# Kernel optimization log

Measured on AMD Instinct MI355X. Metric: run time of the kernel, lower is better.

## Reference

```python
import jax, jax.numpy as jnp
from jax import lax
import numpy as np

B, T, H, A, C = 32, 4096, 512, 512, 32  # batch, enc frames, hidden, attn_size, conv_size


def setup_inputs() -> dict:
    key = jax.random.key(0)
    ks = jax.random.split(key, 10)
    return {
        "decoder_output": jax.random.normal(ks[0], (B, 1, H), jnp.float32),
        "encoder_outputs": jax.random.normal(ks[1], (B, T, H), jnp.float32),
        "last_alignment": jax.random.uniform(ks[2], (B, T), jnp.float32),
        "conv_w": jax.random.normal(ks[3], (C, 1, 3), jnp.float32) * 0.1,   # Conv1d(1->C, k=3)
        "conv_b": jax.random.normal(ks[4], (C,), jnp.float32) * 0.1,
        "W": jax.random.normal(ks[5], (A, H), jnp.float32) * (1.0 / np.sqrt(H)),
        "V": jax.random.normal(ks[6], (A, H), jnp.float32) * (1.0 / np.sqrt(H)),
        "U": jax.random.normal(ks[7], (A, C), jnp.float32) * (1.0 / np.sqrt(C)),
        "b": jax.random.uniform(ks[8], (A,), jnp.float32, -0.1, 0.1),
        "w": jax.random.normal(ks[9], (A,), jnp.float32) * (1.0 / np.sqrt(A)),
    }


def reference(decoder_output, encoder_outputs, last_alignment, conv_w, conv_b, W, V, U, b, w):
    # location conv: [B,1,T] -> [B,C,T], kernel 3, padding 1
    conv = lax.conv_general_dilated(
        last_alignment[:, None, :], conv_w,
        window_strides=(1,), padding=[(1, 1)],
        dimension_numbers=("NCH", "OIH", "NCH"))
    conv_feat = (conv + conv_b[None, :, None]).transpose(0, 2, 1)  # [B,T,C]

    dec_proj = jnp.einsum("blh,ah->bla", decoder_output, W)        # [B,1,A]
    enc_proj = jnp.einsum("bth,ah->bta", encoder_outputs, V)       # [B,T,A]
    loc_proj = jnp.einsum("btc,ac->bta", conv_feat, U)             # [B,T,A]

    scores = jnp.einsum("bta,a->bt", jnp.tanh(dec_proj + enc_proj + loc_proj + b), w)  # [B,T]
    alignment = jax.nn.softmax(scores, axis=-1)                    # [B,T]
    output = jnp.einsum("bt,bth->bh", alignment, encoder_outputs)  # [B,H]
    return output, alignment
```

## Files before the change

### kernel.cpp

```cpp
#include <hip/hip_runtime.h>
#include <hip/hip_bf16.h>

#define B_ 32
#define T_ 4096
#define H_ 512
#define A_ 512
#define C_ 32
#define KTOT 544
#define NKS  (KTOT / 32)
#define TT   128

typedef float f32x4 __attribute__((ext_vector_type(4)));
typedef __bf16 bf16x8 __attribute__((ext_vector_type(8)));
typedef __bf16 bf16x4 __attribute__((ext_vector_type(4)));

__device__ inline float fast_tanh(float x) {
    float t = __expf(2.0f * x);
    return 1.0f - 2.0f / (t + 1.0f);
}

__device__ __forceinline__ void async16(const void* g, void* l) {
    __builtin_amdgcn_global_load_lds(
        (const __attribute__((address_space(1))) unsigned int*)g,
        (__attribute__((address_space(3))) unsigned int*)l, 16, 0, 0);
}

__global__ __launch_bounds__(256) void prep_kernel(
    const float* __restrict__ dec, const float* __restrict__ W,
    const float* __restrict__ bvec, const float* __restrict__ V,
    const float* __restrict__ U,
    float* __restrict__ dpb, __bf16* __restrict__ Vsall) {
    int id = blockIdx.x * 256 + threadIdx.x;
    const int N1 = B_ * A_;
    const int N2 = A_ * H_;
    if (id < N1) {
        int b = id / A_, a = id % A_;
        const float* dr = dec + b * H_;
        const float* wr = W + (size_t)a * H_;
        float s = 0.f;
        #pragma unroll 8
        for (int h = 0; h < H_; ++h) s += dr[h] * wr[h];
        dpb[id] = s + bvec[a];
    } else if (id < N1 + N2) {
        int e = id - N1;
        int a = e >> 9, k = e & 511;
        Vsall[((k >> 3) * A_ + a) * 8 + (k & 7)] = (__bf16)V[(size_t)a * H_ + k];
    } else {
        int e = id - N1 - N2;
        int a = e >> 5, c = e & 31;
        int k = H_ + c;
        Vsall[((k >> 3) * A_ + a) * 8 + (k & 7)] = (__bf16)U[a * C_ + c];
    }
}

__global__ __launch_bounds__(1024) void scores_mfma(
    const float* __restrict__ enc, const float* __restrict__ align,
    const float* __restrict__ conv_w, const float* __restrict__ conv_b,
    const __bf16* __restrict__ Vsall, const float* __restrict__ dpb,
    const float* __restrict__ wvec, float* __restrict__ scores) {
    const int t0 = blockIdx.x * TT;
    const int b  = blockIdx.y;
    const int tid = threadIdx.x;
    const int lane = tid & 63, wid = tid >> 6;
    const int row0 = lane & 15;
    const int kg   = lane >> 4;
    const int wq   = wid & 3;
    const int wr   = wid >> 2;
    const int wcol = wq * 128;

    __shared__ char smem[114688];
    float* spart = (float*)smem;

    const float* encb = enc + ((size_t)b * T_ + t0) * H_;
    const int arow = tid >> 3;
    const int akq  = tid & 7;
    const int aswz = ((arow >> 1) & 3) << 1;
    const int awbyte = arow * 64 + ((akq ^ aswz) << 3);

    int arbyte[2];
    #pragma unroll
    for (int m = 0; m < 2; ++m) {
        int row = wr * 32 + m * 16 + row0;
        int rs = ((row >> 1) & 3) << 1;
        arbyte[m] = row * 64 + (((kg << 1) ^ rs) << 3);
    }

    f32x4 areg[2];
    float cx0 = 0.f, cx1 = 0.f, cx2 = 0.f;

    #pragma unroll
    for (int s = 0; s < 2; ++s) {
        char* bdst = smem + 16384 + s * 32768;
        #pragma unroll
        for (int i = 0; i < 2; ++i) {
            int u = i * 1024 + tid;
            async16(Vsall + (size_t)s * 16384 + (size_t)u * 8, bdst + u * 16);
        }
    }
    {
        f32x4 a0 = *reinterpret_cast<const f32x4*>(encb + arow * H_ + akq * 4);
        areg[1]  = *reinterpret_cast<const f32x4*>(encb + arow * H_ + 32 + akq * 4);
        bf16x4 v;
        v[0] = (__bf16)a0.x; v[1] = (__bf16)a0.y; v[2] = (__bf16)a0.z; v[3] = (__bf16)a0.w;
        *reinterpret_cast<bf16x4*>(smem + awbyte) = v;
    }
    asm volatile("s_waitcnt vmcnt(0) lgkmcnt(0)" ::: "memory");
    __builtin_amdgcn_sched_barrier(0);
    __builtin_amdgcn_s_barrier();

    f32x4 acc[2][8];
    #pragma unroll
    for (int m = 0; m < 2; ++m)
        #pragma unroll
        for (int n = 0; n < 8; ++n) acc[m][n] = (f32x4){0.f, 0.f, 0.f, 0.f};

    #pragma unroll
    for (int ks = 0; ks < NKS; ++ks) {
        if (ks + 2 <= NKS - 1) {
            char* bdst = smem + 16384 + ((ks + 2) % 3) * 32768;
            const __bf16* src = Vsall + (size_t)(ks + 2) * 16384;
            #pragma unroll
            for (int i = 0; i < 2; ++i) {
                int u = i * 1024 + tid;
                async16(src + (size_t)u * 8, bdst + u * 16);
            }
            if (ks + 2 < NKS - 1) {
                areg[ks & 1] = *reinterpret_cast<const f32x4*>(
                    encb + arow * H_ + (ks + 2) * 32 + akq * 4);
            } else {
                int t = t0 + arow;
                int tm = (t > 0) ? t - 1 : 0;
                int tp = (t + 1 < T_) ? t + 1 : T_ - 1;
                cx0 = align[(size_t)b * T_ + tm];
                cx1 = align[(size_t)b * T_ + t];
                cx2 = align[(size_t)b * T_ + tp];
                if (t == 0) cx0 = 0.f;
                if (t + 1 == T_) cx2 = 0.f;
            }
        }

        char* Ard = smem + (ks & 1) * 8192;
        bf16x8 afrag[2];
        #pragma unroll
        for (int m = 0; m < 2; ++m)
            afrag[m] = *reinterpret_cast<const bf16x8*>(Ard + arbyte[m]);
        const __bf16* bp = (const __bf16*)(smem + 16384 + (ks % 3) * 32768) + kg * (A_ * 8);
        #pragma unroll
        for (int n = 0; n < 8; ++n) {
            bf16x8 bfrag = *reinterpret_cast<const bf16x8*>(bp + (wcol + n * 16 + row0) * 8);
            acc[0][n] = __builtin_amdgcn_mfma_f32_16x16x32_bf16(afrag[0], bfrag, acc[0][n], 0, 0, 0);
            acc[1][n] = __builtin_amdgcn_mfma_f32_16x16x32_bf16(afrag[1], bfrag, acc[1][n], 0, 0, 0);
        }

        if (ks + 1 <= NKS - 1) {
            bf16x4 v;
            if (ks + 1 < NKS - 1) {
                f32x4 a = areg[(ks + 1) & 1];
                v[0] = (__bf16)a.x; v[1] = (__bf16)a.y; v[2] = (__bf16)a.z; v[3] = (__bf16)a.w;
            } else {
                #pragma unroll
                for (int e = 0; e < 4; ++e) {
                    int c = akq * 4 + e;
                    v[e] = (__bf16)(conv_b[c] + conv_w[c * 3] * cx0
                                  + conv_w[c * 3 + 1] * cx1 + conv_w[c * 3 + 2] * cx2);
                }
            }
            char* Adst = smem + ((ks + 1) & 1) * 8192;
            *reinterpret_cast<bf16x4*>(Adst + awbyte) = v;
        }

        if (ks < 14) {
            asm volatile("s_waitcnt vmcnt(3) lgkmcnt(0)" ::: "memory");
        } else if (ks == 14) {
            asm volatile("s_waitcnt vmcnt(5) lgkmcnt(0)" ::: "memory");
        } else if (ks == 15) {
            asm volatile("s_waitcnt vmcnt(0) lgkmcnt(0)" ::: "memory");
        }
        if (ks < NKS - 1) {
            __builtin_amdgcn_sched_barrier(0);
            __builtin_amdgcn_s_barrier();
        }
    }
    __syncthreads();

    float dval[8], wv[8];
    #pragma unroll
    for (int n = 0; n < 8; ++n) {
        int a = wcol + n * 16 + row0;
        dval[n] = dpb[b * A_ + a];
        wv[n]   = wvec[a];
    }
    #pragma unroll
    for (int m = 0; m < 2; ++m) {
        float rs[4] = {0.f, 0.f, 0.f, 0.f};
        #pragma unroll
        for (int n = 0; n < 8; ++n) {
            #pragma unroll
            for (int j = 0; j < 4; ++j) {
                float x = acc[m][n][j] + dval[n];
                rs[j] += fast_tanh(x) * wv[n];
            }
        }
        #pragma unroll
        for (int j = 0; j < 4; ++j) {
            float v = rs[j];
            v += __shfl_xor(v, 1);
            v += __shfl_xor(v, 2);
            v += __shfl_xor(v, 4);
            v += __shfl_xor(v, 8);
            if (row0 == 0) spart[wq * TT + wr * 32 + m * 16 + kg * 4 + j] = v;
        }
    }
    __syncthreads();
    if (tid < TT) {
        float s = spart[0 * TT + tid] + spart[1 * TT + tid]
                + spart[2 * TT + tid] + spart[3 * TT + tid];
        scores[b * T_ + t0 + tid] = s;
    }
}

__global__ __launch_bounds__(256) void softmax_k(
    const float* __restrict__ scores, float* __restrict__ out_align) {
    int b = blockIdx.x;
    int tid = threadIdx.x;
    __shared__ float redm[4];
    __shared__ float reds[4];
    float local[16];
    float mx = -1e30f;
    #pragma unroll
    for (int i = 0; i < 16; ++i) {
        float s = scores[b * T_ + tid + i * 256];
        local[i] = s;
        mx = fmaxf(mx, s);
    }
    for (int off = 32; off >= 1; off >>= 1) mx = fmaxf(mx, __shfl_xor(mx, off));
    if ((tid & 63) == 0) redm[tid >> 6] = mx;
    __syncthreads();
    mx = fmaxf(fmaxf(redm[0], redm[1]), fmaxf(redm[2], redm[3]));
    float sum = 0.f;
    #pragma unroll
    for (int i = 0; i < 16; ++i) { local[i] = __expf(local[i] - mx); sum += local[i]; }
    for (int off = 32; off >= 1; off >>= 1) sum += __shfl_xor(sum, off);
    if ((tid & 63) == 0) reds[tid >> 6] = sum;
    __syncthreads();
    sum = reds[0] + reds[1] + reds[2] + reds[3];
    float inv = 1.0f / sum;
    #pragma unroll
    for (int i = 0; i < 16; ++i)
        out_align[b * T_ + tid + i * 256] = local[i] * inv;
}

__global__ __launch_bounds__(512) void pout_k(
    const float* __restrict__ enc, const float* __restrict__ alpha,
    float* __restrict__ pout) {
    int chunk = blockIdx.x;
    int b = blockIdx.y;
    int tid = threadIdx.x;
    int t0 = chunk * 512;
    __shared__ float as[512];
    as[tid] = alpha[b * T_ + t0 + tid];
    __syncthreads();
    float acc = 0.f;
    const float* ep = enc + ((size_t)b * T_ + t0) * H_ + tid;
    #pragma unroll 4
    for (int t = 0; t < 512; ++t) acc += as[t] * ep[(size_t)t * H_];
    pout[((size_t)b * 8 + chunk) * H_ + tid] = acc;
}

__global__ __launch_bounds__(512) void combine_k(
    const float* __restrict__ pout, float* __restrict__ out) {
    int b = blockIdx.x; int h = threadIdx.x;
    float s = 0.f;
    #pragma unroll
    for (int c = 0; c < 8; ++c) s += pout[((size_t)b * 8 + c) * H_ + h];
    out[b * H_ + h] = s;
}

extern "C" void kernel_launch(void* const* d_in, const int* in_sizes, int n_in,
                              void* d_out, int out_size, void* d_ws, size_t ws_size,
                              hipStream_t stream) {
    const float* dec    = (const float*)d_in[0];
    const float* enc    = (const float*)d_in[1];
    const float* align  = (const float*)d_in[2];
    const float* conv_w = (const float*)d_in[3];
    const float* conv_b = (const float*)d_in[4];
    const float* W      = (const float*)d_in[5];
    const float* V      = (const float*)d_in[6];
    const float* U      = (const float*)d_in[7];
    const float* bvec   = (const float*)d_in[8];
    const float* wvec   = (const float*)d_in[9];
    float* out       = (float*)d_out;
    float* out_align = out + B_ * H_;

    char* ws = (char*)d_ws;
    float*  dpb    = (float*)(ws);
    float*  scores = (float*)(ws + (64 << 10));
    float*  pout   = (float*)(ws + (576 << 10));
    __bf16* Vsall  = (__bf16*)(ws + (1088 << 10));

    prep_kernel<<<(B_ * A_ + A_ * H_ + A_ * C_) / 256, 256, 0, stream>>>(
        dec, W, bvec, V, U, dpb, Vsall);
    scores_mfma<<<dim3(T_ / TT, B_), 1024, 0, stream>>>(enc, align, conv_w, conv_b,
                                                        Vsall, dpb, wvec, scores);
    softmax_k<<<B_, 256, 0, stream>>>(scores, out_align);
    pout_k<<<dim3(8, B_), 512, 0, stream>>>(enc, out_align, pout);
    combine_k<<<B_, 512, 0, stream>>>(pout, out);
}
```

Baseline: 193.6 us.

## Split scores kernel into producer and consumer waves with smaller T tile

Restructures the MFMA scores kernel into 8 consumer waves that only run MFMAs and 4 producer waves that issue the async loads of the V/U weight slices and convert the encoder rows to bf16 into LDS. The T tile is halved to 64 rows, so each consumer wave owns a 64-wide column slice of A and a 4x4 accumulator block. The goal is to hide global-load latency behind matrix math through warp specialization. In exchange, every block re-streams the full bf16 weight matrix for only 64 rows, which doubles total weight traffic from L2. Blocks also get smaller, and the launch count doubles.

```diff
diff --git a/kernel.cpp b/kernel.cpp
--- a/kernel.cpp
+++ b/kernel.cpp
@@ -8,11 +8,10 @@
 #define C_ 32
 #define KTOT 544
 #define NKS  (KTOT / 32)
-#define TT   128
+#define TT   64
 
 typedef float f32x4 __attribute__((ext_vector_type(4)));
 typedef __bf16 bf16x8 __attribute__((ext_vector_type(8)));
-typedef __bf16 bf16x4 __attribute__((ext_vector_type(4)));
 
 __device__ inline float fast_tanh(float x) {
     float t = __expf(2.0f * x);
@@ -53,7 +52,7 @@
     }
 }
 
-__global__ __launch_bounds__(1024) void scores_mfma(
+__global__ __launch_bounds__(768) void scores_mfma(
     const float* __restrict__ enc, const float* __restrict__ align,
     const float* __restrict__ conv_w, const float* __restrict__ conv_b,
     const __bf16* __restrict__ Vsall, const float* __restrict__ dpb,
@@ -64,157 +63,173 @@
     const int lane = tid & 63, wid = tid >> 6;
     const int row0 = lane & 15;
     const int kg   = lane >> 4;
-    const int wq   = wid & 3;
-    const int wr   = wid >> 2;
-    const int wcol = wq * 128;
-
-    __shared__ char smem[114688];
+    const bool is_consumer = (wid < 8);
+    const int ptid = tid - 512;
+
+    __shared__ char smem[8192 + 3 * 32768];
     float* spart = (float*)smem;
 
     const float* encb = enc + ((size_t)b * T_ + t0) * H_;
-    const int arow = tid >> 3;
-    const int akq  = tid & 7;
-    const int aswz = ((arow >> 1) & 3) << 1;
-    const int awbyte = arow * 64 + ((akq ^ aswz) << 3);
-
-    int arbyte[2];
-    #pragma unroll
-    for (int m = 0; m < 2; ++m) {
-        int row = wr * 32 + m * 16 + row0;
-        int rs = ((row >> 1) & 3) << 1;
-        arbyte[m] = row * 64 + (((kg << 1) ^ rs) << 3);
-    }
+
+    const int arow = (tid - 512) >> 2;
+    const int akq  = tid & 3;
+    const int ag   = ((tid - 512) ^ (((tid - 512) >> 4) & 7));
+    int arbyte[4];
+    #pragma unroll
+    for (int m = 0; m < 4; ++m) {
+        int row = m * 16 + row0;
+        int u = row * 4 + kg;
+        int g = u ^ ((u >> 4) & 7);
+        arbyte[m] = g * 16;
+    }
+    const int brbase = (kg * 512 + wid * 64 + row0) * 16;
 
     f32x4 areg[2];
     float cx0 = 0.f, cx1 = 0.f, cx2 = 0.f;
 
-    #pragma unroll
-    for (int s = 0; s < 2; ++s) {
-        char* bdst = smem + 16384 + s * 32768;
-        #pragma unroll
-        for (int i = 0; i < 2; ++i) {
-            int u = i * 1024 + tid;
-            async16(Vsall + (size_t)s * 16384 + (size_t)u * 8, bdst + u * 16);
+    if (!is_consumer) {
+        #pragma unroll
+        for (int s = 0; s < 2; ++s) {
+            char* bdst = smem + 8192 + s * 32768;
+            const __bf16* src = Vsall + (size_t)s * 16384;
+            #pragma unroll
+            for (int i = 0; i < 8; ++i) {
+                int u = i * 256 + ptid;
+                async16(src + (size_t)u * 8, bdst + u * 16);
+            }
         }
-    }
-    {
-        f32x4 a0 = *reinterpret_cast<const f32x4*>(encb + arow * H_ + akq * 4);
-        areg[1]  = *reinterpret_cast<const f32x4*>(encb + arow * H_ + 32 + akq * 4);
-        bf16x4 v;
-        v[0] = (__bf16)a0.x; v[1] = (__bf16)a0.y; v[2] = (__bf16)a0.z; v[3] = (__bf16)a0.w;
-        *reinterpret_cast<bf16x4*>(smem + awbyte) = v;
-    }
-    asm volatile("s_waitcnt vmcnt(0) lgkmcnt(0)" ::: "memory");
-    __builtin_amdgcn_sched_barrier(0);
-    __builtin_amdgcn_s_barrier();
-
-    f32x4 acc[2][8];
-    #pragma unroll
-    for (int m = 0; m < 2; ++m)
-        #pragma unroll
-        for (int n = 0; n < 8; ++n) acc[m][n] = (f32x4){0.f, 0.f, 0.f, 0.f};
+        const float* p0 = encb + (size_t)arow * H_ + akq * 8;
+        f32x4 lo = *reinterpret_cast<const f32x4*>(p0);
+        f32x4 hi = *reinterpret_cast<const f32x4*>(p0 + 4);
+        areg[1] = *reinterpret_cast<const f32x4*>(p0 + 32);
+        bf16x8 v;
+        v[0]=(__bf16)lo.x; v[1]=(__bf16)lo.y; v[2]=(__bf16)lo.z; v[3]=(__bf16)lo.w;
+        v[4]=(__bf16)hi.x; v[5]=(__bf16)hi.y; v[6]=(__bf16)hi.z; v[7]=(__bf16)hi.w;
+        *reinterpret_cast<bf16x8*>(smem + ag * 16) = v;
+    }
+    f32x4 areg1b;
+    if (!is_consumer) {
+        const float* p1 = encb + (size_t)arow * H_ + 32 + akq * 8;
+        areg[1] = *reinterpret_cast<const f32x4*>(p1);
+        areg1b  = *reinterpret_cast<const f32x4*>(p1 + 4);
+    }
+    __syncthreads();
+
+    f32x4 acc[4][4];
+    #pragma unroll
+    for (int m = 0; m < 4; ++m)
+        #pragma unroll
+        for (int n = 0; n < 4; ++n) acc[m][n] = (f32x4){0.f, 0.f, 0.f, 0.f};
+
+    f32x4 aregb[2];
+    aregb[1] = areg1b;
 
     #pragma unroll
     for (int ks = 0; ks < NKS; ++ks) {
-        if (ks + 2 <= NKS - 1) {
-            char* bdst = smem + 16384 + ((ks + 2) % 3) * 32768;
-            const __bf16* src = Vsall + (size_t)(ks + 2) * 16384;
-            #pragma unroll
-            for (int i = 0; i < 2; ++i) {
-                int u = i * 1024 + tid;
-                async16(src + (size_t)u * 8, bdst + u * 16);
-            }
-            if (ks + 2 < NKS - 1) {
-                areg[ks & 1] = *reinterpret_cast<const f32x4*>(
-                    encb + arow * H_ + (ks + 2) * 32 + akq * 4);
+        if (is_consumer) {
+            char* Ard = smem + (ks & 1) * 4096;
+            const char* Brd = smem + 8192 + (ks % 3) * 32768;
+            bf16x8 afrag[4];
+            #pragma unroll
+            for (int m = 0; m < 4; ++m)
+                afrag[m] = *reinterpret_cast<const bf16x8*>(Ard + arbyte[m]);
+            #pragma unroll
+            for (int n = 0; n < 4; ++n) {
+                bf16x8 bfrag = *reinterpret_cast<const bf16x8*>(Brd + brbase + n * 256);
+                #pragma unroll
+                for (int m = 0; m < 4; ++m)
+                    acc[m][n] = __builtin_amdgcn_mfma_f32_16x16x32_bf16(afrag[m], bfrag, acc[m][n], 0, 0, 0);
+            }
+        } else {
+            if (ks + 2 <= NKS - 1) {
+                char* bdst = smem + 8192 + ((ks + 2) % 3) * 32768;
+                const __bf16* src = Vsall + (size_t)(ks + 2) * 16384;
+                #pragma unroll
+                for (int i = 0; i < 8; ++i) {
+                    int u = i * 256 + ptid;
+                    async16(src + (size_t)u * 8, bdst + u * 16);
+                }
+                if (ks + 2 < NKS - 1) {
+                    const float* p = encb + (size_t)arow * H_ + (ks + 2) * 32 + akq * 8;
+                    areg[ks & 1]  = *reinterpret_cast<const f32x4*>(p);
+                    aregb[ks & 1] = *reinterpret_cast<const f32x4*>(p + 4);
+                } else {
+                    int t = t0 + arow;
+                    int tm = (t > 0) ? t - 1 : 0;
+                    int tp = (t + 1 < T_) ? t + 1 : T_ - 1;
+                    cx0 = align[(size_t)b * T_ + tm];
+                    cx1 = align[(size_t)b * T_ + t];
+                    cx2 = align[(size_t)b * T_ + tp];
+                    if (t == 0) cx0 = 0.f;
+                    if (t + 1 == T_) cx2 = 0.f;
+                }
+            }
+            if (ks + 1 <= NKS - 1) {
+                bf16x8 v;
+                if (ks + 1 < NKS - 1) {
+                    f32x4 lo = areg[(ks + 1) & 1];
+                    f32x4 hi = aregb[(ks + 1) & 1];
+                    v[0]=(__bf16)lo.x; v[1]=(__bf16)lo.y; v[2]=(__bf16)lo.z; v[3]=(__bf16)lo.w;
+                    v[4]=(__bf16)hi.x; v[5]=(__bf16)hi.y; v[6]=(__bf16)hi.z; v[7]=(__bf16)hi.w;
+                } else {
+                    #pragma unroll
+                    for (int e = 0; e < 8; ++e) {
+                        int c = akq * 8 + e;
+                        v[e] = (__bf16)(conv_b[c] + conv_w[c * 3] * cx0
+                                      + conv_w[c * 3 + 1] * cx1 + conv_w[c * 3 + 2] * cx2);
+                    }
+                }
+                char* Adst = smem + ((ks + 1) & 1) * 4096;
+                *reinterpret_cast<bf16x8*>(Adst + ag * 16) = v;
+            }
+            if (ks < 14) {
+                asm volatile("s_waitcnt vmcnt(10) lgkmcnt(0)" ::: "memory");
+            } else if (ks == 14) {
+                asm volatile("s_waitcnt vmcnt(11) lgkmcnt(0)" ::: "memory");
             } else {
-                int t = t0 + arow;
-                int tm = (t > 0) ? t - 1 : 0;
-                int tp = (t + 1 < T_) ? t + 1 : T_ - 1;
-                cx0 = align[(size_t)b * T_ + tm];
-                cx1 = align[(size_t)b * T_ + t];
-                cx2 = align[(size_t)b * T_ + tp];
-                if (t == 0) cx0 = 0.f;
-                if (t + 1 == T_) cx2 = 0.f;
-            }
+                asm volatile("s_waitcnt vmcnt(0) lgkmcnt(0)" ::: "memory");
+            }
+            __builtin_amdgcn_sched_barrier(0);
         }
-
-        char* Ard = smem + (ks & 1) * 8192;
-        bf16x8 afrag[2];
-        #pragma unroll
-        for (int m = 0; m < 2; ++m)
-            afrag[m] = *reinterpret_cast<const bf16x8*>(Ard + arbyte[m]);
-        const __bf16* bp = (const __bf16*)(smem + 16384 + (ks % 3) * 32768) + kg * (A_ * 8);
-        #pragma unroll
-        for (int n = 0; n < 8; ++n) {
-            bf16x8 bfrag = *reinterpret_cast<const bf16x8*>(bp + (wcol + n * 16 + row0) * 8);
-            acc[0][n] = __builtin_amdgcn_mfma_f32_16x16x32_bf16(afrag[0], bfrag, acc[0][n], 0, 0, 0);
-            acc[1][n] = __builtin_amdgcn_mfma_f32_16x16x32_bf16(afrag[1], bfrag, acc[1][n], 0, 0, 0);
+        __builtin_amdgcn_s_barrier();
+    }
+    __syncthreads();
+
+    if (is_consumer) {
+        float dval[4], wv[4];
+        #pragma unroll
+        for (int n = 0; n < 4; ++n) {
+            int a = wid * 64 + n * 16 + row0;
+            dval[n] = dpb[b * A_ + a];
+            wv[n]   = wvec[a];
         }
-
-        if (ks + 1 <= NKS - 1) {
-            bf16x4 v;
-            if (ks + 1 < NKS - 1) {
-                f32x4 a = areg[(ks + 1) & 1];
-                v[0] = (__bf16)a.x; v[1] = (__bf16)a.y; v[2] = (__bf16)a.z; v[3] = (__bf16)a.w;
-            } else {
+        #pragma unroll
+        for (int m = 0; m < 4; ++m) {
+            float rs[4] = {0.f, 0.f, 0.f, 0.f};
+            #pragma unroll
+            for (int n = 0; n < 4; ++n) {
                 #pragma unroll
-                for (int e = 0; e < 4; ++e) {
-                    int c = akq * 4 + e;
-                    v[e] = (__bf16)(conv_b[c] + conv_w[c * 3] * cx0
-                                  + conv_w[c * 3 + 1] * cx1 + conv_w[c * 3 + 2] * cx2);
+                for (int j = 0; j < 4; ++j) {
+                    float x = acc[m][n][j] + dval[n];
+                    rs[j] += fast_tanh(x) * wv[n];
                 }
             }
-            char* Adst = smem + ((ks + 1) & 1) * 8192;
-            *reinterpret_cast<bf16x4*>(Adst + awbyte) = v;
+            #pragma unroll
+            for (int j = 0; j < 4; ++j) {
+                float v = rs[j];
+                v += __shfl_xor(v, 1);
+                v += __shfl_xor(v, 2);
+                v += __shfl_xor(v, 4);
+                v += __shfl_xor(v, 8);
+                if (row0 == 0) spart[wid * TT + m * 16 + kg * 4 + j] = v;
+            }
         }
-
-        if (ks < 14) {
-            asm volatile("s_waitcnt vmcnt(3) lgkmcnt(0)" ::: "memory");
-        } else if (ks == 14) {
-            asm volatile("s_waitcnt vmcnt(5) lgkmcnt(0)" ::: "memory");
-        } else if (ks == 15) {
-            asm volatile("s_waitcnt vmcnt(0) lgkmcnt(0)" ::: "memory");
-        }
-        if (ks < NKS - 1) {
-            __builtin_amdgcn_sched_barrier(0);
-            __builtin_amdgcn_s_barrier();
-        }
-    }
-    __syncthreads();
-
-    float dval[8], wv[8];
-    #pragma unroll
-    for (int n = 0; n < 8; ++n) {
-        int a = wcol + n * 16 + row0;
-        dval[n] = dpb[b * A_ + a];
-        wv[n]   = wvec[a];
-    }
-    #pragma unroll
-    for (int m = 0; m < 2; ++m) {
-        float rs[4] = {0.f, 0.f, 0.f, 0.f};
-        #pragma unroll
-        for (int n = 0; n < 8; ++n) {
-            #pragma unroll
-            for (int j = 0; j < 4; ++j) {
-                float x = acc[m][n][j] + dval[n];
-                rs[j] += fast_tanh(x) * wv[n];
-            }
-        }
-        #pragma unroll
-        for (int j = 0; j < 4; ++j) {
-            float v = rs[j];
-            v += __shfl_xor(v, 1);
-            v += __shfl_xor(v, 2);
-            v += __shfl_xor(v, 4);
-            v += __shfl_xor(v, 8);
-            if (row0 == 0) spart[wq * TT + wr * 32 + m * 16 + kg * 4 + j] = v;
-        }
     }
     __syncthreads();
     if (tid < TT) {
-        float s = spart[0 * TT + tid] + spart[1 * TT + tid]
-                + spart[2 * TT + tid] + spart[3 * TT + tid];
+        float s = 0.f;
+        #pragma unroll
+        for (int w = 0; w < 8; ++w) s += spart[w * TT + tid];
         scores[b * T_ + t0 + tid] = s;
     }
 }
@@ -300,8 +315,8 @@
 
     prep_kernel<<<(B_ * A_ + A_ * H_ + A_ * C_) / 256, 256, 0, stream>>>(
         dec, W, bvec, V, U, dpb, Vsall);
-    scores_mfma<<<dim3(T_ / TT, B_), 1024, 0, stream>>>(enc, align, conv_w, conv_b,
-                                                        Vsall, dpb, wvec, scores);
+    scores_mfma<<<dim3(T_ / TT, B_), 768, 0, stream>>>(enc, align, conv_w, conv_b,
+                                                       Vsall, dpb, wvec, scores);
     softmax_k<<<B_, 256, 0, stream>>>(scores, out_align);
     pout_k<<<dim3(8, B_), 512, 0, stream>>>(enc, out_align, pout);
     combine_k<<<B_, 512, 0, stream>>>(pout, out);
```

Measured after the change: 230.5 us. 1.19x slower.
